# Optimization experiments

Hardware: AMD Instinct MI355X
Metric: run time of the kernel (lower is better)

The kernel has to match this reference:

```python
import jax, jax.numpy as jnp
import numpy as np

NEG_INF = -1e30
EPS = 1e-7  # keras epsilon used by K.ctc_batch_cost


def setup_inputs() -> dict:
    key = jax.random.key(0)
    k1, k2 = jax.random.split(key)
    B, T, C, L = 1024, 256, 128, 32
    logits = jax.random.normal(k1, (B, T, C), dtype=jnp.float32)
    y_pred = jax.nn.softmax(logits, axis=-1)  # ctc_batch_cost expects probabilities
    y_true = jax.random.randint(k2, (B, L), 0, 126, dtype=jnp.int64)
    return {"y_true": y_true, "y_pred": y_pred}


def _ctc_batch_cost(y_true, y_pred):
    # Faithful to K.ctc_batch_cost with input_length=T, label_length=L, blank=C-1
    B, T, C = y_pred.shape
    L = y_true.shape[1]
    blank = C - 1
    S = 2 * L + 1
    logp = jnp.log(y_pred + EPS)  # [B,T,C]

    # extended label sequence: blank, l0, blank, l1, ..., blank  -> [B,S]
    ext = jnp.full((B, S), blank, dtype=jnp.int32)
    ext = ext.at[:, 1::2].set(y_true.astype(jnp.int32))

    # emission log-probs along extended labels: [B,T,S]
    lp_ext = jnp.take_along_axis(logp, ext[:, None, :], axis=2)

    # s-2 skip allowed only for non-blank labels differing from label two back
    is_blank = ext == blank
    same2 = jnp.concatenate(
        [jnp.ones((B, 2), bool), ext[:, 2:] == ext[:, :-2]], axis=1)
    skip_add = jnp.where(is_blank | same2, NEG_INF, 0.0)  # [B,S]

    alpha0 = jnp.full((B, S), NEG_INF, dtype=logp.dtype)
    alpha0 = alpha0.at[:, 0].set(lp_ext[:, 0, 0])
    alpha0 = alpha0.at[:, 1].set(lp_ext[:, 0, 1])

    def shift(x, n):
        return jnp.pad(x, ((0, 0), (n, 0)), constant_values=NEG_INF)[:, :S]

    def step(alpha, lp_t):
        a0 = alpha
        a1 = shift(alpha, 1)
        a2 = jnp.maximum(shift(alpha, 2) + skip_add, NEG_INF)
        m = jnp.maximum(jnp.maximum(a0, a1), a2)
        lse = m + jnp.log(jnp.exp(a0 - m) + jnp.exp(a1 - m) + jnp.exp(a2 - m))
        new = jnp.maximum(lse + lp_t, NEG_INF)
        return new, None

    lp_ext_t = jnp.swapaxes(lp_ext, 0, 1)  # [T,B,S]
    alpha_T, _ = jax.lax.scan(step, alpha0, lp_ext_t[1:])
    final = jnp.logaddexp(alpha_T[:, S - 1], alpha_T[:, S - 2])  # [B]
    return -final[:, None]  # [B,1] like ctc_batch_cost


def reference(y_true, y_pred):
    return _ctc_batch_cost(y_true, y_pred)
```

## Files before the change

### kernel.cpp

```cpp
#include <hip/hip_runtime.h>
#include <hip/hip_bf16.h>


#define CTC_B 1024
#define CTC_T 256
#define CTC_C 128
#define CTC_L 32
#define CTC_BLANK 127
#define CTC_EPS 1e-7f

#define RSTRIDE 34

#define DPP_WAVE_SHL1 0x130
#define DPP_WAVE_SHR1 0x138

__device__ __forceinline__ double bperm_f64(int addr, double v) {
    union { double d; int i[2]; } u; u.d = v;
    int x = __builtin_amdgcn_ds_bpermute(addr, u.i[0]);
    int y = __builtin_amdgcn_ds_bpermute(addr, u.i[1]);
    union { int i[2]; double d; } r; r.i[0] = x; r.i[1] = y;
    return r.d;
}

__device__ __forceinline__ double dpp_shr1_f64(double v) {
    union { double d; int i[2]; } u; u.d = v;
    int x = __builtin_amdgcn_update_dpp(0, u.i[0], DPP_WAVE_SHR1, 0xF, 0xF, true);
    int y = __builtin_amdgcn_update_dpp(0, u.i[1], DPP_WAVE_SHR1, 0xF, 0xF, true);
    union { int i[2]; double d; } r; r.i[0] = x; r.i[1] = y;
    return r.d;
}

__device__ __forceinline__ double dpp_shl1_f64(double v) {
    union { double d; int i[2]; } u; u.d = v;
    int x = __builtin_amdgcn_update_dpp(0, u.i[0], DPP_WAVE_SHL1, 0xF, 0xF, true);
    int y = __builtin_amdgcn_update_dpp(0, u.i[1], DPP_WAVE_SHL1, 0xF, 0xF, true);
    union { int i[2]; double d; } r; r.i[0] = x; r.i[1] = y;
    return r.d;
}

__device__ __forceinline__ double bcast0_f64(double v) {
    union { double d; int i[2]; } u; u.d = v;
    int x = __builtin_amdgcn_readfirstlane(u.i[0]);
    int y = __builtin_amdgcn_readfirstlane(u.i[1]);
    union { int i[2]; double d; } r; r.i[0] = x; r.i[1] = y;
    return r.d;
}

__global__ __launch_bounds__(256) void ctc_loss_kernel(
    const int* __restrict__ y_true,
    const float* __restrict__ y_pred,
    float* __restrict__ out)
{
    __shared__ float lp[CTC_T * RSTRIDE];

    const int b = blockIdx.x;
    const int tid = threadIdx.x;
    const int lane = tid & 63;
    const int wave = tid >> 6;

    const float* yp = y_pred + (size_t)b * CTC_T * CTC_C;

    int lbl = CTC_BLANK;
    if (lane < CTC_L) lbl = y_true[b * CTC_L + lane];

    {
        const int t0 = wave * 64;
        #pragma unroll 8
        for (int k = 0; k < 64; ++k) {
            int t = t0 + k;
            float p = yp[t * CTC_C + lbl];
            float v = (lane == 33) ? 0.0f : (p + CTC_EPS) * 128.0f;
            if (lane <= 33) lp[t * RSTRIDE + lane] = v;
        }
    }
    __syncthreads();

    if (wave != 0) return;

    double skip = 0.0;
    if (lane >= 1 && lane < CTC_L) {
        if (y_true[b * CTC_L + lane - 1] != lbl) skip = 1.0;
    }
    double skipn = 0.0;
    if (lane <= 30) {
        if (y_true[b * CTC_L + lane + 1] != lbl) skipn = 1.0;
    } else if (lane == 32) {
        skipn = 1.0;
    }

    const int lidx = (lane < 32) ? lane : 32;
    const int pv_idx = (lane < 32) ? lane : 33;
    const int tn = (lane <= 30) ? (lane + 1)
                 : (lane == 31) ? 33
                 : (lane == 32) ? 0
                 : 32;
    const int pbi = (lane == 32) ? 33 : 32;
    const bool is32 = (lane == 32);

    double lo = 0.0, hi = 0.0;
    if (lane == 0) {
        lo = (double)lp[32];
        hi = (double)lp[0];
    }
    double a = 0.0, bb = 0.0;
    if (lane == 31) { a = 1.0; bb = 1.0; }

    for (int k = 0; k < 127; ++k) {
        const int tf = 1 + k;
        const int tb = 255 - k;
        float pvf  = lp[tf * RSTRIDE + pv_idx];
        float pbf  = lp[tf * RSTRIDE + 32];
        float paf  = lp[tb * RSTRIDE + lidx];
        float pa1f = lp[tb * RSTRIDE + tn];
        float pbbf = lp[tb * RSTRIDE + pbi];

        double ph  = dpp_shr1_f64(hi);
        double a1s = dpp_shl1_f64(a);
        double a1  = is32 ? bcast0_f64(a) : a1s;

        double nl = (lo + ph) * (double)pbf;
        double nh = (hi + lo + skip * ph) * (double)pvf;
        double v  = (double)pa1f * a1;
        double u  = (double)pbbf * bb;
        double nb = u + v;
        double na = fma((double)paf, a, fma(skipn, v, u));

        lo = nl; hi = nh; a = na; bb = nb;
    }

    {
        const int tb = 128;
        float paf  = lp[tb * RSTRIDE + lidx];
        float pa1f = lp[tb * RSTRIDE + tn];
        float pbbf = lp[tb * RSTRIDE + pbi];
        double a1s = dpp_shl1_f64(a);
        double a1  = is32 ? bcast0_f64(a) : a1s;
        double v  = (double)pa1f * a1;
        double u  = (double)pbbf * bb;
        double nb = u + v;
        double na = fma((double)paf, a, fma(skipn, v, u));
        a = na; bb = nb;
    }

    double beA = bperm_f64(32 << 2, a);
    double beB = bperm_f64(((lane + 63) & 63) << 2, bb);
    double be = (lane == 0) ? beA : beB;
    double partial = (lane <= 32) ? (lo * be + hi * a) : 0.0;
    #pragma unroll
    for (int off = 32; off >= 1; off >>= 1)
        partial += __shfl_down(partial, off);
    if (lane == 0) {
        out[b] = (float)(1242.1197475634219 - log(partial));
    }
}

extern "C" void kernel_launch(void* const* d_in, const int* in_sizes, int n_in,
                              void* d_out, int out_size, void* d_ws, size_t ws_size,
                              hipStream_t stream) {
    const int*   y_true = (const int*)d_in[0];
    const float* y_pred = (const float*)d_in[1];
    float*       out    = (float*)d_out;

    ctc_loss_kernel<<<CTC_B, 256, 0, stream>>>(y_true, y_pred, out);
}
```

Baseline: 203.5 us.

## Drop LDS staging and stream emissions from global with register double-buffering

```diff
diff --git a/kernel.cpp b/kernel.cpp
--- a/kernel.cpp
+++ b/kernel.cpp
@@ -8,8 +8,6 @@
 #define CTC_L 32
 #define CTC_BLANK 127
 #define CTC_EPS 1e-7f
-
-#define RSTRIDE 34
 
 #define DPP_WAVE_SHL1 0x130
 #define DPP_WAVE_SHR1 0x138
@@ -38,6 +36,10 @@
     return r.d;
 }
 
+__device__ __forceinline__ int dpp_shl1_i32(int v) {
+    return __builtin_amdgcn_update_dpp(0, v, DPP_WAVE_SHL1, 0xF, 0xF, true);
+}
+
 __device__ __forceinline__ double bcast0_f64(double v) {
     union { double d; int i[2]; } u; u.d = v;
     int x = __builtin_amdgcn_readfirstlane(u.i[0]);
@@ -46,36 +48,18 @@
     return r.d;
 }
 
-__global__ __launch_bounds__(256) void ctc_loss_kernel(
+__global__ __launch_bounds__(64) void ctc_loss_kernel(
     const int* __restrict__ y_true,
     const float* __restrict__ y_pred,
     float* __restrict__ out)
 {
-    __shared__ float lp[CTC_T * RSTRIDE];
-
     const int b = blockIdx.x;
-    const int tid = threadIdx.x;
-    const int lane = tid & 63;
-    const int wave = tid >> 6;
+    const int lane = threadIdx.x;
 
     const float* yp = y_pred + (size_t)b * CTC_T * CTC_C;
 
     int lbl = CTC_BLANK;
     if (lane < CTC_L) lbl = y_true[b * CTC_L + lane];
-
-    {
-        const int t0 = wave * 64;
-        #pragma unroll 8
-        for (int k = 0; k < 64; ++k) {
-            int t = t0 + k;
-            float p = yp[t * CTC_C + lbl];
-            float v = (lane == 33) ? 0.0f : (p + CTC_EPS) * 128.0f;
-            if (lane <= 33) lp[t * RSTRIDE + lane] = v;
-        }
-    }
-    __syncthreads();
-
-    if (wave != 0) return;
 
     double skip = 0.0;
     if (lane >= 1 && lane < CTC_L) {
@@ -87,52 +71,89 @@
     } else if (lane == 32) {
         skipn = 1.0;
     }
+    const bool is32 = (lane == 32);
 
-    const int lidx = (lane < 32) ? lane : 32;
-    const int pv_idx = (lane < 32) ? lane : 33;
-    const int tn = (lane <= 30) ? (lane + 1)
-                 : (lane == 31) ? 33
-                 : (lane == 32) ? 0
-                 : 32;
-    const int pbi = (lane == 32) ? 33 : 32;
-    const bool is32 = (lane == 32);
+    const int col_a = (lane < 32) ? lbl : CTC_BLANK;
+    const int lbl_next = dpp_shl1_i32(lbl);
+    const int lbl0 = __builtin_amdgcn_readfirstlane(lbl);
+    const int col_n = (lane <= 31) ? lbl_next
+                    : (lane == 32) ? lbl0
+                    : CTC_BLANK;
 
     double lo = 0.0, hi = 0.0;
     if (lane == 0) {
-        lo = (double)lp[32];
-        hi = (double)lp[0];
+        lo = (double)((yp[CTC_BLANK] + CTC_EPS) * 128.0f);
+        hi = (double)((yp[lbl] + CTC_EPS) * 128.0f);
     }
     double a = 0.0, bb = 0.0;
     if (lane == 31) { a = 1.0; bb = 1.0; }
 
-    for (int k = 0; k < 127; ++k) {
-        const int tf = 1 + k;
-        const int tb = 255 - k;
-        float pvf  = lp[tf * RSTRIDE + pv_idx];
-        float pbf  = lp[tf * RSTRIDE + 32];
-        float paf  = lp[tb * RSTRIDE + lidx];
-        float pa1f = lp[tb * RSTRIDE + tn];
-        float pbbf = lp[tb * RSTRIDE + pbi];
-
-        double ph  = dpp_shr1_f64(hi);
-        double a1s = dpp_shl1_f64(a);
-        double a1  = is32 ? bcast0_f64(a) : a1s;
-
-        double nl = (lo + ph) * (double)pbf;
-        double nh = (hi + lo + skip * ph) * (double)pvf;
-        double v  = (double)pa1f * a1;
-        double u  = (double)pbbf * bb;
-        double nb = u + v;
-        double na = fma((double)paf, a, fma(skipn, v, u));
-
-        lo = nl; hi = nh; a = na; bb = nb;
+#define STEPK(Ltf, Lta, Ltn) {                                      \
+        float vtf = ((Ltf) + CTC_EPS) * 128.0f;                     \
+        float vta = ((Lta) + CTC_EPS) * 128.0f;                     \
+        float vtn = ((Ltn) + CTC_EPS) * 128.0f;                     \
+        float pbf = __int_as_float(                                 \
+            __builtin_amdgcn_readlane(__float_as_int(vtf), 32));    \
+        float pbbb = __int_as_float(                                \
+            __builtin_amdgcn_readlane(__float_as_int(vta), 63));    \
+        float pvf  = (lane < 32) ? vtf : 0.0f;                      \
+        float paf  = vta;                                           \
+        float pa1f = (lane == 31) ? 0.0f : vtn;                     \
+        float pbbf = is32 ? 0.0f : pbbb;                            \
+        double ph  = dpp_shr1_f64(hi);                              \
+        double a1s = dpp_shl1_f64(a);                               \
+        double a1  = is32 ? bcast0_f64(a) : a1s;                    \
+        double nl = (lo + ph) * (double)pbf;                        \
+        double nh = (hi + lo + skip * ph) * (double)pvf;            \
+        double v  = (double)pa1f * a1;                              \
+        double u  = (double)pbbf * bb;                              \
+        double nb = u + v;                                          \
+        double na = fma((double)paf, a, fma(skipn, v, u));          \
+        lo = nl; hi = nh; a = na; bb = nb;                          \
     }
 
+#define LOADG(dtf, dta, dtn, g) {                                   \
+        _Pragma("unroll")                                           \
+        for (int s = 0; s < 8; ++s) {                               \
+            const int k = 8 * (g) + s;                              \
+            const float* rf = yp + (size_t)(1 + k) * CTC_C;         \
+            const float* rb = yp + (size_t)(255 - k) * CTC_C;       \
+            dtf[s] = rf[col_a];                                     \
+            dta[s] = rb[col_a];                                     \
+            dtn[s] = rb[col_n];                                     \
+        }                                                           \
+    }
+
+    float ctf[8], cta[8], ctn[8];
+    float ntf[8], nta[8], ntn[8];
+
+    LOADG(ctf, cta, ctn, 0);
+
+    for (int g = 0; g < 15; ++g) {
+        LOADG(ntf, nta, ntn, g + 1);
+        __builtin_amdgcn_sched_barrier(0);
+        #pragma unroll
+        for (int s = 0; s < 8; ++s)
+            STEPK(ctf[s], cta[s], ctn[s]);
+        __builtin_amdgcn_sched_barrier(0);
+        #pragma unroll
+        for (int s = 0; s < 8; ++s) {
+            ctf[s] = ntf[s]; cta[s] = nta[s]; ctn[s] = ntn[s];
+        }
+    }
+
+    #pragma unroll
+    for (int s = 0; s < 7; ++s)
+        STEPK(ctf[s], cta[s], ctn[s]);
+
     {
-        const int tb = 128;
-        float paf  = lp[tb * RSTRIDE + lidx];
-        float pa1f = lp[tb * RSTRIDE + tn];
-        float pbbf = lp[tb * RSTRIDE + pbi];
+        float vta = (cta[7] + CTC_EPS) * 128.0f;
+        float vtn = (ctn[7] + CTC_EPS) * 128.0f;
+        float pbbb = __int_as_float(
+            __builtin_amdgcn_readlane(__float_as_int(vta), 63));
+        float paf  = vta;
+        float pa1f = (lane == 31) ? 0.0f : vtn;
+        float pbbf = is32 ? 0.0f : pbbb;
         double a1s = dpp_shl1_f64(a);
         double a1  = is32 ? bcast0_f64(a) : a1s;
         double v  = (double)pa1f * a1;
@@ -141,6 +162,8 @@
         double na = fma((double)paf, a, fma(skipn, v, u));
         a = na; bb = nb;
     }
+#undef STEPK
+#undef LOADG
 
     double beA = bperm_f64(32 << 2, a);
     double beB = bperm_f64(((lane + 63) & 63) << 2, bb);
@@ -161,5 +184,5 @@
     const float* y_pred = (const float*)d_in[1];
     float*       out    = (float*)d_out;
 
-    ctc_loss_kernel<<<CTC_B, 256, 0, stream>>>(y_true, y_pred, out);
+    ctc_loss_kernel<<<CTC_B, 64, 0, stream>>>(y_true, y_pred, out);
 }
```

After: 193.2 us. 5.1% less time.

## Split forward/backward recursions across two waves with streamed register-buffered global loads

Applied to the files above, without the earlier changes.

```diff
diff --git a/kernel.cpp b/kernel.cpp
--- a/kernel.cpp
+++ b/kernel.cpp
@@ -1,5 +1,4 @@
 #include <hip/hip_runtime.h>
-#include <hip/hip_bf16.h>
 
 
 #define CTC_B 1024
@@ -9,18 +8,8 @@
 #define CTC_BLANK 127
 #define CTC_EPS 1e-7f
 
-#define RSTRIDE 34
-
 #define DPP_WAVE_SHL1 0x130
 #define DPP_WAVE_SHR1 0x138
-
-__device__ __forceinline__ double bperm_f64(int addr, double v) {
-    union { double d; int i[2]; } u; u.d = v;
-    int x = __builtin_amdgcn_ds_bpermute(addr, u.i[0]);
-    int y = __builtin_amdgcn_ds_bpermute(addr, u.i[1]);
-    union { int i[2]; double d; } r; r.i[0] = x; r.i[1] = y;
-    return r.d;
-}
 
 __device__ __forceinline__ double dpp_shr1_f64(double v) {
     union { double d; int i[2]; } u; u.d = v;
@@ -46,12 +35,42 @@
     return r.d;
 }
 
-__global__ __launch_bounds__(256) void ctc_loss_kernel(
+#define GLOAD(dst, voff, base, OFFSTR)                              \
+    asm volatile("global_load_dword %0, %1, %2 offset:" OFFSTR      \
+                 : "=v"(dst) : "v"(voff), "s"(base) : "memory")
+
+#define VM8  do { asm volatile("s_waitcnt vmcnt(8)" ::: "memory");  \
+                  __builtin_amdgcn_sched_barrier(0); } while (0)
+#define VM0  do { asm volatile("s_waitcnt vmcnt(0)" ::: "memory");  \
+                  __builtin_amdgcn_sched_barrier(0); } while (0)
+
+#define FISSUE(buf, voff) {                 \
+    GLOAD(buf[0], voff, yp, "0");           \
+    GLOAD(buf[1], voff, yp, "512");         \
+    GLOAD(buf[2], voff, yp, "1024");        \
+    GLOAD(buf[3], voff, yp, "1536");        \
+    GLOAD(buf[4], voff, yp, "2048");        \
+    GLOAD(buf[5], voff, yp, "2560");        \
+    GLOAD(buf[6], voff, yp, "3072");        \
+    GLOAD(buf[7], voff, yp, "3584"); }
+
+#define BISSUE(buf, voff) {                 \
+    GLOAD(buf[0], voff, yp, "0");           \
+    GLOAD(buf[1], voff, yp, "-512");        \
+    GLOAD(buf[2], voff, yp, "-1024");       \
+    GLOAD(buf[3], voff, yp, "-1536");       \
+    GLOAD(buf[4], voff, yp, "-2048");       \
+    GLOAD(buf[5], voff, yp, "-2560");       \
+    GLOAD(buf[6], voff, yp, "-3072");       \
+    GLOAD(buf[7], voff, yp, "-3584"); }
+
+__global__ __launch_bounds__(128) void ctc_loss_kernel(
     const int* __restrict__ y_true,
     const float* __restrict__ y_pred,
     float* __restrict__ out)
 {
-    __shared__ float lp[CTC_T * RSTRIDE];
+    __shared__ double sA[64];
+    __shared__ double sB[64];
 
     const int b = blockIdx.x;
     const int tid = threadIdx.x;
@@ -62,95 +81,122 @@
 
     int lbl = CTC_BLANK;
     if (lane < CTC_L) lbl = y_true[b * CTC_L + lane];
-
-    {
-        const int t0 = wave * 64;
-        #pragma unroll 8
-        for (int k = 0; k < 64; ++k) {
-            int t = t0 + k;
-            float p = yp[t * CTC_C + lbl];
-            float v = (lane == 33) ? 0.0f : (p + CTC_EPS) * 128.0f;
-            if (lane <= 33) lp[t * RSTRIDE + lane] = v;
-        }
+    const int col_a = (lane < 32) ? lbl : CTC_BLANK;
+    const bool is32 = (lane == 32);
+
+    double lo = 0.0, hi = 0.0;
+
+    if (wave == 0) {
+        double skip = 0.0;
+        if (lane >= 1 && lane < CTC_L) {
+            if (y_true[b * CTC_L + lane - 1] != lbl) skip = 1.0;
+        }
+        if (lane == 0) {
+            lo = (double)((yp[CTC_BLANK] + CTC_EPS) * 128.0f);
+            hi = (double)((yp[lbl] + CTC_EPS) * 128.0f);
+        }
+
+#define FSTEP(Lt) {                                                         \
+        float vtf = ((Lt) + CTC_EPS) * 128.0f;                              \
+        float pbf = __int_as_float(                                         \
+            __builtin_amdgcn_readlane(__float_as_int(vtf), 32));            \
+        float pvf = (lane < 32) ? vtf : 0.0f;                               \
+        double ph = dpp_shr1_f64(hi);                                       \
+        double nl = (lo + ph) * (double)pbf;                                \
+        double nh = (hi + lo + skip * ph) * (double)pvf;                    \
+        lo = nl; hi = nh; }
+
+        float A[8], Bv[8];
+        int voffA = 1 * 512 + col_a * 4;
+        int voffB = 9 * 512 + col_a * 4;
+        FISSUE(A, voffA);  voffA += 8192;
+        FISSUE(Bv, voffB); voffB += 8192;
+        for (int g = 0; g < 14; g += 2) {
+            VM8;
+            FSTEP(A[0]); FSTEP(A[1]); FSTEP(A[2]); FSTEP(A[3]);
+            FSTEP(A[4]); FSTEP(A[5]); FSTEP(A[6]); FSTEP(A[7]);
+            FISSUE(A, voffA); voffA += 8192;
+            VM8;
+            FSTEP(Bv[0]); FSTEP(Bv[1]); FSTEP(Bv[2]); FSTEP(Bv[3]);
+            FSTEP(Bv[4]); FSTEP(Bv[5]); FSTEP(Bv[6]); FSTEP(Bv[7]);
+            FISSUE(Bv, voffB); voffB += 8192;
+        }
+        VM8;
+        FSTEP(A[0]); FSTEP(A[1]); FSTEP(A[2]); FSTEP(A[3]);
+        FSTEP(A[4]); FSTEP(A[5]); FSTEP(A[6]); FSTEP(A[7]);
+        VM0;
+        FSTEP(Bv[0]); FSTEP(Bv[1]); FSTEP(Bv[2]); FSTEP(Bv[3]);
+        FSTEP(Bv[4]); FSTEP(Bv[5]); FSTEP(Bv[6]);
+#undef FSTEP
+    } else {
+        double skipn = 0.0;
+        if (lane <= 30) {
+            if (y_true[b * CTC_L + lane + 1] != lbl) skipn = 1.0;
+        } else if (lane == 32) {
+            skipn = 1.0;
+        }
+        double a = 0.0, bb = 0.0;
+        if (lane == 31) { a = 1.0; bb = 1.0; }
+
+#define BSTEP(Lt) {                                                         \
+        float vta = ((Lt) + CTC_EPS) * 128.0f;                              \
+        float pbbb = __int_as_float(                                        \
+            __builtin_amdgcn_readlane(__float_as_int(vta), 63));            \
+        float sh = __int_as_float(__builtin_amdgcn_update_dpp(              \
+            0, __float_as_int(vta), DPP_WAVE_SHL1, 0xF, 0xF, true));        \
+        float f0 = __int_as_float(                                          \
+            __builtin_amdgcn_readfirstlane(__float_as_int(vta)));           \
+        float pa1f = (lane == 31) ? 0.0f : (is32 ? f0 : sh);                \
+        float paf  = vta;                                                   \
+        float pbbf = is32 ? 0.0f : pbbb;                                    \
+        double a1s = dpp_shl1_f64(a);                                       \
+        double a1  = is32 ? bcast0_f64(a) : a1s;                            \
+        double v  = (double)pa1f * a1;                                      \
+        double u  = (double)pbbf * bb;                                      \
+        double nb = u + v;                                                  \
+        double na = fma((double)paf, a, fma(skipn, v, u));                  \
+        a = na; bb = nb; }
+
+        float A[8], Bv[8];
+        int voffA = 255 * 512 + col_a * 4;
+        int voffB = 247 * 512 + col_a * 4;
+        BISSUE(A, voffA);  voffA -= 8192;
+        BISSUE(Bv, voffB); voffB -= 8192;
+        for (int g = 0; g < 14; g += 2) {
+            VM8;
+            BSTEP(A[0]); BSTEP(A[1]); BSTEP(A[2]); BSTEP(A[3]);
+            BSTEP(A[4]); BSTEP(A[5]); BSTEP(A[6]); BSTEP(A[7]);
+            BISSUE(A, voffA); voffA -= 8192;
+            VM8;
+            BSTEP(Bv[0]); BSTEP(Bv[1]); BSTEP(Bv[2]); BSTEP(Bv[3]);
+            BSTEP(Bv[4]); BSTEP(Bv[5]); BSTEP(Bv[6]); BSTEP(Bv[7]);
+            BISSUE(Bv, voffB); voffB -= 8192;
+        }
+        VM8;
+        BSTEP(A[0]); BSTEP(A[1]); BSTEP(A[2]); BSTEP(A[3]);
+        BSTEP(A[4]); BSTEP(A[5]); BSTEP(A[6]); BSTEP(A[7]);
+        VM0;
+        BSTEP(Bv[0]); BSTEP(Bv[1]); BSTEP(Bv[2]); BSTEP(Bv[3]);
+        BSTEP(Bv[4]); BSTEP(Bv[5]); BSTEP(Bv[6]); BSTEP(Bv[7]);
+#undef BSTEP
+
+        sA[lane] = a;
+        sB[lane] = bb;
     }
+
     __syncthreads();
 
-    if (wave != 0) return;
-
-    double skip = 0.0;
-    if (lane >= 1 && lane < CTC_L) {
-        if (y_true[b * CTC_L + lane - 1] != lbl) skip = 1.0;
-    }
-    double skipn = 0.0;
-    if (lane <= 30) {
-        if (y_true[b * CTC_L + lane + 1] != lbl) skipn = 1.0;
-    } else if (lane == 32) {
-        skipn = 1.0;
-    }
-
-    const int lidx = (lane < 32) ? lane : 32;
-    const int pv_idx = (lane < 32) ? lane : 33;
-    const int tn = (lane <= 30) ? (lane + 1)
-                 : (lane == 31) ? 33
-                 : (lane == 32) ? 0
-                 : 32;
-    const int pbi = (lane == 32) ? 33 : 32;
-    const bool is32 = (lane == 32);
-
-    double lo = 0.0, hi = 0.0;
-    if (lane == 0) {
-        lo = (double)lp[32];
-        hi = (double)lp[0];
-    }
-    double a = 0.0, bb = 0.0;
-    if (lane == 31) { a = 1.0; bb = 1.0; }
-
-    for (int k = 0; k < 127; ++k) {
-        const int tf = 1 + k;
-        const int tb = 255 - k;
-        float pvf  = lp[tf * RSTRIDE + pv_idx];
-        float pbf  = lp[tf * RSTRIDE + 32];
-        float paf  = lp[tb * RSTRIDE + lidx];
-        float pa1f = lp[tb * RSTRIDE + tn];
-        float pbbf = lp[tb * RSTRIDE + pbi];
-
-        double ph  = dpp_shr1_f64(hi);
-        double a1s = dpp_shl1_f64(a);
-        double a1  = is32 ? bcast0_f64(a) : a1s;
-
-        double nl = (lo + ph) * (double)pbf;
-        double nh = (hi + lo + skip * ph) * (double)pvf;
-        double v  = (double)pa1f * a1;
-        double u  = (double)pbbf * bb;
-        double nb = u + v;
-        double na = fma((double)paf, a, fma(skipn, v, u));
-
-        lo = nl; hi = nh; a = na; bb = nb;
-    }
-
-    {
-        const int tb = 128;
-        float paf  = lp[tb * RSTRIDE + lidx];
-        float pa1f = lp[tb * RSTRIDE + tn];
-        float pbbf = lp[tb * RSTRIDE + pbi];
-        double a1s = dpp_shl1_f64(a);
-        double a1  = is32 ? bcast0_f64(a) : a1s;
-        double v  = (double)pa1f * a1;
-        double u  = (double)pbbf * bb;
-        double nb = u + v;
-        double na = fma((double)paf, a, fma(skipn, v, u));
-        a = na; bb = nb;
-    }
-
-    double beA = bperm_f64(32 << 2, a);
-    double beB = bperm_f64(((lane + 63) & 63) << 2, bb);
-    double be = (lane == 0) ? beA : beB;
-    double partial = (lane <= 32) ? (lo * be + hi * a) : 0.0;
-    #pragma unroll
-    for (int off = 32; off >= 1; off >>= 1)
-        partial += __shfl_down(partial, off);
-    if (lane == 0) {
-        out[b] = (float)(1242.1197475634219 - log(partial));
+    if (wave == 0) {
+        double aown = sA[lane];
+        double beB  = sB[(lane + 63) & 63];
+        double be   = (lane == 0) ? sA[32] : beB;
+        double partial = (lane <= 32) ? (lo * be + hi * aown) : 0.0;
+        #pragma unroll
+        for (int off = 32; off >= 1; off >>= 1)
+            partial += __shfl_down(partial, off);
+        if (lane == 0) {
+            out[b] = (float)(1242.1197475634219 - log(partial));
+        }
     }
 }
 
@@ -161,5 +207,5 @@
     const float* y_pred = (const float*)d_in[1];
     float*       out    = (float*)d_out;
 
-    ctc_loss_kernel<<<CTC_B, 256, 0, stream>>>(y_true, y_pred, out);
-}
+    ctc_loss_kernel<<<CTC_B, 128, 0, stream>>>(y_true, y_pred, out);
+}
```

Measured after the change: 193.4 us. 1.05x faster.
